# Kernel optimization log

Hardware: AMD Instinct MI355X
Metric: run time of the kernel (lower is better)

The kernel has to match this reference:

```python
import jax, jax.numpy as jnp
import numpy as np

N_NODES = 100000
N_EDGES = 1600000
D_IN = 64
D_OUT = 64


def setup_inputs() -> dict:
    key = jax.random.key(0)
    k1, k2, k3, k4 = jax.random.split(key, 4)
    x = jax.random.normal(k1, (N_NODES, D_IN), dtype=jnp.float32)
    W = jax.random.normal(k2, (D_OUT, D_IN), dtype=jnp.float32) * 0.1
    b = jax.random.normal(k3, (D_OUT,), dtype=jnp.float32) * 0.1
    edge_index = jax.random.randint(k4, (2, N_EDGES), 0, N_NODES, dtype=jnp.int64 if jax.config.jax_enable_x64 else jnp.int32)
    return {"x": x, "W": W, "b": b, "edge_index": edge_index}


def reference(x, W, b, edge_index):
    N = x.shape[0]
    # add self loops
    loop = jnp.arange(N, dtype=edge_index.dtype)
    src = jnp.concatenate([edge_index[0], loop])  # row: source nodes
    dst = jnp.concatenate([edge_index[1], loop])  # col: target nodes
    E = src.shape[0]

    # linear transform
    h = x @ W.T + b  # [N, D_OUT]

    # degree over source (row) indices, as in the original message()
    ones = jnp.ones((E,), dtype=h.dtype)
    deg = jax.ops.segment_sum(ones, src, num_segments=N)  # [N]
    deg_inv_sqrt = jnp.where(deg > 0, jax.lax.rsqrt(jnp.maximum(deg, 1.0)), 0.0)
    norm = deg_inv_sqrt[src] * deg_inv_sqrt[dst]  # [E]

    # gather-scale messages, then scatter-mean into targets
    msg = norm[:, None] * h[src]  # [E, D_OUT]
    agg_sum = jax.ops.segment_sum(msg, dst, num_segments=N)  # [N, D_OUT]
    cnt = jax.ops.segment_sum(ones, dst, num_segments=N)  # [N]
    out = agg_sum / jnp.maximum(cnt, 1.0)[:, None]
    return out
```

## Files before the change

### kernel.cpp

```cpp
#include <hip/hip_runtime.h>
#include <hip/hip_fp16.h>

#define N_D 64
#define PB_D 5
#define PSZ_D 32
#define CAP_D 768
#define SCAP  1024
#define GCAP  (SCAP / 8)
#define PB_S 7
#define PSZ_S 128
#define CAP_S 3072

__global__ __launch_bounds__(1024) void scatter_kernel(const int* __restrict__ src,
                                                       const int* __restrict__ dst,
                                                       int* __restrict__ cursorD,
                                                       int* __restrict__ cursorS,
                                                       unsigned* __restrict__ epart,
                                                       unsigned char* __restrict__ spart,
                                                       int E, int PD, int PS) {
    extern __shared__ int sh[];
    int* hD = sh;
    int* hS = sh + PD;
    int* bD = sh + PD + PS;
    int* bS = sh + 2 * PD + PS;
    int t = threadIdx.x;
    for (int i = t; i < PD + PS; i += 1024) sh[i] = 0;
    __syncthreads();
    const int4* src4 = (const int4*)src;
    const int4* dst4 = (const int4*)dst;
    int E4 = E >> 2;
    int per = (E4 + gridDim.x - 1) / gridDim.x;
    int beg = blockIdx.x * per, end = min(E4, beg + per);
    bool tailblk = (blockIdx.x == 0);
    for (int e = beg + t; e < end; e += 1024) {
        int4 d = dst4[e];
        int4 s = src4[e];
        atomicAdd(&hD[d.x >> PB_D], 1);
        atomicAdd(&hD[d.y >> PB_D], 1);
        atomicAdd(&hD[d.z >> PB_D], 1);
        atomicAdd(&hD[d.w >> PB_D], 1);
        atomicAdd(&hS[s.x >> PB_S], 1);
        atomicAdd(&hS[s.y >> PB_S], 1);
        atomicAdd(&hS[s.z >> PB_S], 1);
        atomicAdd(&hS[s.w >> PB_S], 1);
    }
    if (tailblk) {
        for (int e = (E4 << 2) + t; e < E; e += 1024) {
            atomicAdd(&hD[dst[e] >> PB_D], 1);
            atomicAdd(&hS[src[e] >> PB_S], 1);
        }
    }
    __syncthreads();
    for (int p = t; p < PD; p += 1024) {
        int hd = hD[p];
        if (hd) {
            int r = atomicAdd(&cursorD[p], hd);
            if (r > CAP_D - hd) r = max(CAP_D - hd, 0);
            bD[p] = r;
        }
        hD[p] = 0;
    }
    for (int p = t; p < PS; p += 1024) {
        int hs_ = hS[p];
        if (hs_) {
            int r = atomicAdd(&cursorS[p], hs_);
            if (r > CAP_S - hs_) r = max(CAP_S - hs_, 0);
            bS[p] = r;
        }
        hS[p] = 0;
    }
    __syncthreads();
    for (int e = beg + t; e < end; e += 1024) {
        int4 dv = dst4[e];
        int4 sv = src4[e];
        int ds_[4] = {dv.x, dv.y, dv.z, dv.w};
        int ss_[4] = {sv.x, sv.y, sv.z, sv.w};
#pragma unroll
        for (int k = 0; k < 4; k++) {
            int d = ds_[k], s0 = ss_[k];
            int pd = d >> PB_D, ps = s0 >> PB_S;
            int od = atomicAdd(&hD[pd], 1);
            epart[(size_t)pd * CAP_D + bD[pd] + od] =
                ((unsigned)s0 << PB_D) | (unsigned)(d & (PSZ_D - 1));
            int os = atomicAdd(&hS[ps], 1);
            spart[(size_t)ps * CAP_S + bS[ps] + os] = (unsigned char)(s0 & (PSZ_S - 1));
        }
    }
    if (tailblk) {
        for (int e = (E4 << 2) + t; e < E; e += 1024) {
            int d = dst[e], s0 = src[e];
            int pd = d >> PB_D, ps = s0 >> PB_S;
            int od = atomicAdd(&hD[pd], 1);
            epart[(size_t)pd * CAP_D + bD[pd] + od] =
                ((unsigned)s0 << PB_D) | (unsigned)(d & (PSZ_D - 1));
            int os = atomicAdd(&hS[ps], 1);
            spart[(size_t)ps * CAP_S + bS[ps] + os] = (unsigned char)(s0 & (PSZ_S - 1));
        }
    }
}

#define LROWS 128
__global__ __launch_bounds__(256) void linear_kernel(const float* __restrict__ x,
                                                     const float* __restrict__ W,
                                                     const float* __restrict__ b,
                                                     const unsigned char* __restrict__ spart,
                                                     const int* __restrict__ cursorS,
                                                     float* __restrict__ dis,
                                                     __half* __restrict__ hs, int N) {
    __shared__ float xs[LROWS][N_D + 1];
    __shared__ float Wt[N_D][N_D + 4];
    __shared__ float bs[N_D];
    __shared__ int ohist[PSZ_S];
    __shared__ float disS[PSZ_S];

    int tid = threadIdx.x;
    int p = blockIdx.x;
    if (p == 0 && tid < 32) ((int*)hs)[(size_t)N * 32 + tid] = 0;
    if (tid < PSZ_S) ohist[tid] = 0;
    for (int i = tid; i < N_D * N_D; i += 256) {
        int o = i >> 6, k = i & 63;
        Wt[k][o] = W[i];
    }
    if (tid < N_D) bs[tid] = b[tid];
    __syncthreads();

    {
        size_t sbase = (size_t)p * CAP_S;
        int len = min(cursorS[p], CAP_S);
        const unsigned* sp4 = (const unsigned*)(spart + sbase);
        int n4 = len >> 2;
        for (int i = tid; i < n4; i += 256) {
            unsigned v = sp4[i];
            atomicAdd(&ohist[v & 127], 1);
            atomicAdd(&ohist[(v >> 8) & 127], 1);
            atomicAdd(&ohist[(v >> 16) & 127], 1);
            atomicAdd(&ohist[(v >> 24) & 127], 1);
        }
        for (int i = (n4 << 2) + tid; i < len; i += 256)
            atomicAdd(&ohist[spart[sbase + i]], 1);
    }

    int row0 = p * LROWS;
    const float4* x4 = (const float4*)(x + (size_t)row0 * N_D);
    const int n4x = LROWS * N_D / 4;
    if (row0 + LROWS <= N) {
        for (int i = tid; i < n4x; i += 256) {
            float4 v = x4[i];
            int r = i >> 4, kq = (i & 15) << 2;
            xs[r][kq] = v.x; xs[r][kq + 1] = v.y; xs[r][kq + 2] = v.z; xs[r][kq + 3] = v.w;
        }
    } else {
        for (int i = tid; i < n4x; i += 256) {
            int r = i >> 4, kq = (i & 15) << 2;
            float4 v = make_float4(0.f, 0.f, 0.f, 0.f);
            if (row0 + r < N) v = x4[i];
            xs[r][kq] = v.x; xs[r][kq + 1] = v.y; xs[r][kq + 2] = v.z; xs[r][kq + 3] = v.w;
        }
    }
    __syncthreads();

    if (tid < PSZ_S) {
        float dv = rsqrtf((float)(ohist[tid] + 1));
        disS[tid] = dv;
        int node = row0 + tid;
        if (node < N) dis[node] = dv;
    }
    __syncthreads();

    int tc = tid >> 5;
    int tr = tid & 31;
    float acc[4][8];
#pragma unroll
    for (int j = 0; j < 4; j++)
#pragma unroll
        for (int i = 0; i < 8; i++) acc[j][i] = 0.f;

#pragma unroll 4
    for (int k = 0; k < N_D; k++) {
        float4 w0 = *(const float4*)&Wt[k][tc * 8];
        float4 w1 = *(const float4*)&Wt[k][tc * 8 + 4];
        float wv[8] = {w0.x, w0.y, w0.z, w0.w, w1.x, w1.y, w1.z, w1.w};
        float xv[4];
#pragma unroll
        for (int j = 0; j < 4; j++) xv[j] = xs[tr + 32 * j][k];
#pragma unroll
        for (int j = 0; j < 4; j++)
#pragma unroll
            for (int i = 0; i < 8; i++) acc[j][i] += xv[j] * wv[i];
    }

#pragma unroll
    for (int j = 0; j < 4; j++) {
        int row = row0 + tr + 32 * j;
        if (row < N) {
            float dr = disS[tr + 32 * j];
            union { __half h[8]; int4 v; } u;
#pragma unroll
            for (int i = 0; i < 8; i++)
                u.h[i] = __float2half_rn((acc[j][i] + bs[tc * 8 + i]) * dr);
            *(int4*)(hs + (size_t)row * N_D + tc * 8) = u.v;
        }
    }
}

__device__ __forceinline__ void acc8(int4 v, float* a) {
    union { int i; __half2 h; } u;
    float2 f;
    u.i = v.x; f = __half22float2(u.h); a[0] += f.x; a[1] += f.y;
    u.i = v.y; f = __half22float2(u.h); a[2] += f.x; a[3] += f.y;
    u.i = v.z; f = __half22float2(u.h); a[4] += f.x; a[5] += f.y;
    u.i = v.w; f = __half22float2(u.h); a[6] += f.x; a[7] += f.y;
}

__global__ __launch_bounds__(256) void gather_part_kernel(const unsigned* __restrict__ epart,
                                                          const int* __restrict__ cursorD,
                                                          const __half* __restrict__ hs,
                                                          const float* __restrict__ dis,
                                                          float* __restrict__ out, int N) {
    __shared__ unsigned raw[CAP_D];
    __shared__ int sorted[SCAP];
    __shared__ int hist[PSZ_D];
    __shared__ int rs[PSZ_D];
    __shared__ int cur[PSZ_D];
    __shared__ short gnode[GCAP + 8];
    __shared__ float disL[PSZ_D];
    int p = blockIdx.x, t = threadIdx.x;
    if (t < PSZ_D) hist[t] = 0;
    __syncthreads();
    size_t base = (size_t)p * CAP_D;
    int num = min(cursorD[p], CAP_D);
    {
        const uint4* ep4 = (const uint4*)(epart + base);
        int n4 = num >> 2;
        for (int i4 = t; i4 < n4; i4 += 256) {
            uint4 v = ep4[i4];
            ((uint4*)raw)[i4] = v;
            atomicAdd(&hist[v.x & (PSZ_D - 1)], 1);
            atomicAdd(&hist[v.y & (PSZ_D - 1)], 1);
            atomicAdd(&hist[v.z & (PSZ_D - 1)], 1);
            atomicAdd(&hist[v.w & (PSZ_D - 1)], 1);
        }
        for (int i = (n4 << 2) + t; i < num; i += 256) {
            unsigned e = epart[base + i];
            raw[i] = e;
            atomicAdd(&hist[e & (PSZ_D - 1)], 1);
        }
    }
    __syncthreads();
    if (t < PSZ_D) {
        int v = (hist[t] + 8) & ~7;
        int s = v;
#pragma unroll
        for (int off = 1; off < PSZ_D; off <<= 1) {
            int n = __shfl_up(s, off, 64);
            if (t >= off) s += n;
        }
        int ex = s - v;
        rs[t] = ex;
        cur[t] = ex;
        int cnt = hist[t];
        int node = (p << PB_D) + t;
        int pb = ex + cnt;
        int pad = ((cnt + 8) & ~7) - cnt;
        const int ZERO_OFF = N << 7;
        sorted[pb] = (node < N) ? (node << 7) : ZERO_OFF;
        for (int k = 1; k < pad; k++) sorted[pb + k] = ZERO_OFF;
        int g0 = ex >> 3, g1 = (ex + cnt + pad) >> 3;
        for (int G = g0; G < g1; ++G) gnode[G] = (short)t;
        if (t == PSZ_D - 1) gnode[g1] = -1;
        disL[t] = (node < N) ? dis[node] : 0.f;
    }
    __syncthreads();
    for (int i = t; i < num; i += 256) {
        unsigned e = raw[i];
        int pos = atomicAdd(&cur[e & (PSZ_D - 1)], 1);
        sorted[pos] = (int)((e & ~(unsigned)(PSZ_D - 1)) << 2);
    }
    __syncthreads();

    int w = t >> 6, lane = t & 63;
    int g = lane & 7, q = lane >> 3;
    int qb = q << 4;
    const char* hbase = (const char*)hs;
    int r0 = w * 8;
    int rlast = r0 + 7;
    int G = rs[r0] >> 3;
    int gend = (rs[rlast] + ((hist[rlast] + 8) & ~7)) >> 3;
    int r = r0;
    float a[8];
#pragma unroll
    for (int i = 0; i < 8; i++) a[i] = 0.f;

    auto proc = [&](int4 v, int Gi) {
        acc8(v, a);
        int nr = gnode[Gi + 1];
        if (nr != r) {
#pragma unroll
            for (int m = 1; m <= 4; m <<= 1)
#pragma unroll
                for (int i = 0; i < 8; i++) a[i] += __shfl_xor(a[i], m, 64);
            int node = (p << PB_D) + r;
            float scale = disL[r] / (float)(hist[r] + 1);
            if (g == 0 && node < N) {
                float4* op = (float4*)(out + ((size_t)node << 6) + (q << 3));
                op[0] = make_float4(a[0] * scale, a[1] * scale, a[2] * scale, a[3] * scale);
                op[1] = make_float4(a[4] * scale, a[5] * scale, a[6] * scale, a[7] * scale);
            }
#pragma unroll
            for (int i = 0; i < 8; i++) a[i] = 0.f;
            r = nr;
        }
    };

    while (G + 8 <= gend) {
        int o0 = sorted[(G + 0) * 8 + g] + qb;
        int o1 = sorted[(G + 1) * 8 + g] + qb;
        int o2 = sorted[(G + 2) * 8 + g] + qb;
        int o3 = sorted[(G + 3) * 8 + g] + qb;
        int o4 = sorted[(G + 4) * 8 + g] + qb;
        int o5 = sorted[(G + 5) * 8 + g] + qb;
        int o6 = sorted[(G + 6) * 8 + g] + qb;
        int o7 = sorted[(G + 7) * 8 + g] + qb;
        int4 v0 = *(const int4*)(hbase + (size_t)(unsigned)o0);
        int4 v1 = *(const int4*)(hbase + (size_t)(unsigned)o1);
        int4 v2 = *(const int4*)(hbase + (size_t)(unsigned)o2);
        int4 v3 = *(const int4*)(hbase + (size_t)(unsigned)o3);
        int4 v4 = *(const int4*)(hbase + (size_t)(unsigned)o4);
        int4 v5 = *(const int4*)(hbase + (size_t)(unsigned)o5);
        int4 v6 = *(const int4*)(hbase + (size_t)(unsigned)o6);
        int4 v7 = *(const int4*)(hbase + (size_t)(unsigned)o7);
        proc(v0, G + 0);
        proc(v1, G + 1);
        proc(v2, G + 2);
        proc(v3, G + 3);
        proc(v4, G + 4);
        proc(v5, G + 5);
        proc(v6, G + 6);
        proc(v7, G + 7);
        G += 8;
    }
    while (G < gend) {
        int o = sorted[G * 8 + g] + qb;
        int4 v = *(const int4*)(hbase + (size_t)(unsigned)o);
        proc(v, G);
        ++G;
    }
}

extern "C" void kernel_launch(void* const* d_in, const int* in_sizes, int n_in,
                              void* d_out, int out_size, void* d_ws, size_t ws_size,
                              hipStream_t stream) {
    const float* x = (const float*)d_in[0];
    const float* W = (const float*)d_in[1];
    const float* b = (const float*)d_in[2];
    const int* edge_index = (const int*)d_in[3];

    const int N = in_sizes[0] / N_D;
    const int E = in_sizes[3] / 2;
    const int* src = edge_index;
    const int* dst = edge_index + E;
    float* out = (float*)d_out;

    const int PD = (N + PSZ_D - 1) / PSZ_D;
    const int PS = (N + PSZ_S - 1) / PSZ_S;

    char* ws = (char*)d_ws;
    size_t off = 0;
    __half* hs = (__half*)(ws + off);         off += ((size_t)(N + 1) * N_D * sizeof(__half) + 15) & ~15ull;
    float* dis = (float*)(ws + off);          off += (size_t)N * sizeof(float);
    unsigned* epart = (unsigned*)(ws + off);  off += (size_t)PD * CAP_D * sizeof(unsigned);
    unsigned char* spart = (unsigned char*)(ws + off); off += (size_t)PS * CAP_S;
    int* cursorD = (int*)(ws + off);          off += (size_t)PD * sizeof(int);
    int* cursorS = (int*)(ws + off);          off += (size_t)PS * sizeof(int);
    (void)ws_size;

    size_t lds_scat = 2u * (PD + PS) * sizeof(int);

    hipMemsetAsync(cursorD, 0, (size_t)(PD + PS) * sizeof(int), stream);

    scatter_kernel<<<256, 1024, lds_scat, stream>>>(src, dst, cursorD, cursorS,
                                                    epart, spart, E, PD, PS);
    linear_kernel<<<PS, 256, 0, stream>>>(x, W, b, spart, cursorS, dis, hs, N);
    gather_part_kernel<<<PD, 256, 0, stream>>>(epart, cursorD, hs, dis, out, N);
}
```

Measured before the change: 190.0 us.

## Fuse scatter, linear and gather stages into one cooperative persistent kernel

Replaces the memset and three separate kernel launches with a single cooperative kernel that separates the phases with grid.sync and reuses one shared-memory union across them. Cursor zeroing moves inside the kernel, and the histogram pass is split from the reserve pass by a grid barrier. The linear and gather stages become persistent sweeps over partitions, and each 1024-thread block handles eight gather partitions at once through 128-thread sub-groups. The aim is to remove launch gaps and the memset, at the cost of grid-wide barriers, lower occupancy from the large LDS footprint, and possible load imbalance.

```diff
diff --git a/kernel.cpp b/kernel.cpp
--- a/kernel.cpp
+++ b/kernel.cpp
@@ -1,5 +1,8 @@
 #include <hip/hip_runtime.h>
 #include <hip/hip_fp16.h>
+#include <hip/hip_cooperative_groups.h>
+
+namespace cg = cooperative_groups;
 
 #define N_D 64
 #define PB_D 5
@@ -10,340 +13,355 @@
 #define PB_S 7
 #define PSZ_S 128
 #define CAP_S 3072
-
-__global__ __launch_bounds__(1024) void scatter_kernel(const int* __restrict__ src,
-                                                       const int* __restrict__ dst,
-                                                       int* __restrict__ cursorD,
-                                                       int* __restrict__ cursorS,
-                                                       unsigned* __restrict__ epart,
-                                                       unsigned char* __restrict__ spart,
-                                                       int E, int PD, int PS) {
-    extern __shared__ int sh[];
-    int* hD = sh;
-    int* hS = sh + PD;
-    int* bD = sh + PD + PS;
-    int* bS = sh + 2 * PD + PS;
-    int t = threadIdx.x;
-    for (int i = t; i < PD + PS; i += 1024) sh[i] = 0;
-    __syncthreads();
-    const int4* src4 = (const int4*)src;
-    const int4* dst4 = (const int4*)dst;
-    int E4 = E >> 2;
-    int per = (E4 + gridDim.x - 1) / gridDim.x;
-    int beg = blockIdx.x * per, end = min(E4, beg + per);
-    bool tailblk = (blockIdx.x == 0);
-    for (int e = beg + t; e < end; e += 1024) {
-        int4 d = dst4[e];
-        int4 s = src4[e];
-        atomicAdd(&hD[d.x >> PB_D], 1);
-        atomicAdd(&hD[d.y >> PB_D], 1);
-        atomicAdd(&hD[d.z >> PB_D], 1);
-        atomicAdd(&hD[d.w >> PB_D], 1);
-        atomicAdd(&hS[s.x >> PB_S], 1);
-        atomicAdd(&hS[s.y >> PB_S], 1);
-        atomicAdd(&hS[s.z >> PB_S], 1);
-        atomicAdd(&hS[s.w >> PB_S], 1);
+#define LROWS 128
+#define NTHR 1024
+#define PD_C 3125
+#define PS_C 782
+
+struct GatSub {
+    unsigned raw[CAP_D];
+    int sorted[SCAP];
+    int hist[PSZ_D];
+    int rs[PSZ_D];
+    int cur[PSZ_D];
+    short gnode[GCAP + 8];
+    float disL[PSZ_D];
+};
+
+union SharedU {
+    int scat[2 * (PD_C + PS_C)];
+    struct {
+        float xs[LROWS][N_D + 1];
+        float Wt[N_D][N_D + 4];
+        float bs[N_D];
+        int ohist[PSZ_S];
+        float disS[PSZ_S];
+    } lin;
+    struct {
+        GatSub sub[8];
+    } gat;
+};
+
+__global__ __launch_bounds__(NTHR, 8) void fused_kernel(
+    const float* __restrict__ x, const float* __restrict__ W, const float* __restrict__ bias,
+    const int* __restrict__ src, const int* __restrict__ dst, int E, int N, int PD, int PS,
+    unsigned* __restrict__ epart, unsigned char* __restrict__ spart,
+    int* __restrict__ cursorD, int* __restrict__ cursorS,
+    float* __restrict__ dis, __half* __restrict__ hs, float* __restrict__ out) {
+    __shared__ SharedU sh;
+    cg::grid_group grid = cg::this_grid();
+    const int t = threadIdx.x;
+    const int blk = blockIdx.x;
+    const int nb = gridDim.x;
+
+    {
+        int* hD = sh.scat;
+        int* hS = sh.scat + PD;
+        int* bD = sh.scat + PD + PS;
+        int* bS = sh.scat + 2 * PD + PS;
+        for (int i = t; i < PD + PS; i += NTHR) sh.scat[i] = 0;
+        for (int i = blk * NTHR + t; i < PD; i += nb * NTHR) cursorD[i] = 0;
+        for (int i = blk * NTHR + t; i < PS; i += nb * NTHR) cursorS[i] = 0;
+        __syncthreads();
+        const int4* src4 = (const int4*)src;
+        const int4* dst4 = (const int4*)dst;
+        int E4 = E >> 2;
+        int per = (E4 + nb - 1) / nb;
+        int beg = blk * per, end = min(E4, beg + per);
+        bool tailblk = (blk == 0);
+        for (int e = beg + t; e < end; e += NTHR) {
+            int4 d = dst4[e];
+            int4 s = src4[e];
+            atomicAdd(&hD[d.x >> PB_D], 1);
+            atomicAdd(&hD[d.y >> PB_D], 1);
+            atomicAdd(&hD[d.z >> PB_D], 1);
+            atomicAdd(&hD[d.w >> PB_D], 1);
+            atomicAdd(&hS[s.x >> PB_S], 1);
+            atomicAdd(&hS[s.y >> PB_S], 1);
+            atomicAdd(&hS[s.z >> PB_S], 1);
+            atomicAdd(&hS[s.w >> PB_S], 1);
+        }
+        if (tailblk) {
+            for (int e = (E4 << 2) + t; e < E; e += NTHR) {
+                atomicAdd(&hD[dst[e] >> PB_D], 1);
+                atomicAdd(&hS[src[e] >> PB_S], 1);
+            }
+        }
+        __syncthreads();
+        __threadfence();
+        grid.sync();
+        for (int p = t; p < PD; p += NTHR) {
+            int hd = hD[p];
+            if (hd) {
+                int r = atomicAdd(&cursorD[p], hd);
+                if (r > CAP_D - hd) r = max(CAP_D - hd, 0);
+                bD[p] = r;
+            }
+            hD[p] = 0;
+        }
+        for (int p = t; p < PS; p += NTHR) {
+            int hs_ = hS[p];
+            if (hs_) {
+                int r = atomicAdd(&cursorS[p], hs_);
+                if (r > CAP_S - hs_) r = max(CAP_S - hs_, 0);
+                bS[p] = r;
+            }
+            hS[p] = 0;
+        }
+        __syncthreads();
+        for (int e = beg + t; e < end; e += NTHR) {
+            int4 dv = dst4[e];
+            int4 sv = src4[e];
+            int ds_[4] = {dv.x, dv.y, dv.z, dv.w};
+            int ss_[4] = {sv.x, sv.y, sv.z, sv.w};
+#pragma unroll
+            for (int k = 0; k < 4; k++) {
+                int d = ds_[k], s0 = ss_[k];
+                int pd = d >> PB_D, ps = s0 >> PB_S;
+                int od = atomicAdd(&hD[pd], 1);
+                epart[(size_t)pd * CAP_D + bD[pd] + od] =
+                    ((unsigned)s0 << PB_D) | (unsigned)(d & (PSZ_D - 1));
+                int os = atomicAdd(&hS[ps], 1);
+                spart[(size_t)ps * CAP_S + bS[ps] + os] = (unsigned char)(s0 & (PSZ_S - 1));
+            }
+        }
+        if (tailblk) {
+            for (int e = (E4 << 2) + t; e < E; e += NTHR) {
+                int d = dst[e], s0 = src[e];
+                int pd = d >> PB_D, ps = s0 >> PB_S;
+                int od = atomicAdd(&hD[pd], 1);
+                epart[(size_t)pd * CAP_D + bD[pd] + od] =
+                    ((unsigned)s0 << PB_D) | (unsigned)(d & (PSZ_D - 1));
+                int os = atomicAdd(&hS[ps], 1);
+                spart[(size_t)ps * CAP_S + bS[ps] + os] = (unsigned char)(s0 & (PSZ_S - 1));
+            }
+        }
     }
-    if (tailblk) {
-        for (int e = (E4 << 2) + t; e < E; e += 1024) {
-            atomicAdd(&hD[dst[e] >> PB_D], 1);
-            atomicAdd(&hS[src[e] >> PB_S], 1);
+    __threadfence();
+    grid.sync();
+
+    {
+        if (blk == 0 && t < 32) ((int*)hs)[(size_t)N * 32 + t] = 0;
+        for (int i = t; i < N_D * N_D; i += NTHR) {
+            int o = i >> 6, k = i & 63;
+            sh.lin.Wt[k][o] = W[i];
+        }
+        if (t < N_D) sh.lin.bs[t] = bias[t];
+        int sweepsL = (PS + nb - 1) / nb;
+        for (int s = 0; s < sweepsL; s++) {
+            int pt = s * nb + blk;
+            bool act = pt < PS;
+            if (t < PSZ_S) sh.lin.ohist[t] = 0;
+            __syncthreads();
+            int row0 = pt * LROWS;
+            if (act) {
+                size_t sbase = (size_t)pt * CAP_S;
+                int len = min(cursorS[pt], CAP_S);
+                const unsigned* sp4 = (const unsigned*)(spart + sbase);
+                int n4 = len >> 2;
+                for (int i = t; i < n4; i += NTHR) {
+                    unsigned v = sp4[i];
+                    atomicAdd(&sh.lin.ohist[v & 127], 1);
+                    atomicAdd(&sh.lin.ohist[(v >> 8) & 127], 1);
+                    atomicAdd(&sh.lin.ohist[(v >> 16) & 127], 1);
+                    atomicAdd(&sh.lin.ohist[(v >> 24) & 127], 1);
+                }
+                for (int i = (n4 << 2) + t; i < len; i += NTHR)
+                    atomicAdd(&sh.lin.ohist[spart[sbase + i]], 1);
+                const float4* x4 = (const float4*)(x + (size_t)row0 * N_D);
+                for (int i = t; i < LROWS * N_D / 4; i += NTHR) {
+                    int r = i >> 4, kq = (i & 15) << 2;
+                    float4 v = make_float4(0.f, 0.f, 0.f, 0.f);
+                    if (row0 + r < N) v = x4[i];
+                    sh.lin.xs[r][kq] = v.x;
+                    sh.lin.xs[r][kq + 1] = v.y;
+                    sh.lin.xs[r][kq + 2] = v.z;
+                    sh.lin.xs[r][kq + 3] = v.w;
+                }
+            }
+            __syncthreads();
+            if (act && t < PSZ_S) {
+                float dv = 0.f;
+                int node = row0 + t;
+                if (node < N) {
+                    dv = rsqrtf((float)(sh.lin.ohist[t] + 1));
+                    dis[node] = dv;
+                }
+                sh.lin.disS[t] = dv;
+            }
+            __syncthreads();
+            if (act) {
+                int tc = t >> 7;
+                int tr = t & 127;
+                float acc[8];
+#pragma unroll
+                for (int i = 0; i < 8; i++) acc[i] = 0.f;
+#pragma unroll 4
+                for (int k = 0; k < N_D; k++) {
+                    float xv = sh.lin.xs[tr][k];
+                    float4 w0 = *(const float4*)&sh.lin.Wt[k][tc * 8];
+                    float4 w1 = *(const float4*)&sh.lin.Wt[k][tc * 8 + 4];
+                    acc[0] += xv * w0.x; acc[1] += xv * w0.y;
+                    acc[2] += xv * w0.z; acc[3] += xv * w0.w;
+                    acc[4] += xv * w1.x; acc[5] += xv * w1.y;
+                    acc[6] += xv * w1.z; acc[7] += xv * w1.w;
+                }
+                int row = row0 + tr;
+                if (row < N) {
+                    float dr = sh.lin.disS[tr];
+                    union { __half h[8]; int4 v; } u;
+#pragma unroll
+                    for (int i = 0; i < 8; i++)
+                        u.h[i] = __float2half_rn((acc[i] + sh.lin.bs[tc * 8 + i]) * dr);
+                    *(int4*)(hs + (size_t)row * N_D + tc * 8) = u.v;
+                }
+            }
+            __syncthreads();
         }
     }
-    __syncthreads();
-    for (int p = t; p < PD; p += 1024) {
-        int hd = hD[p];
-        if (hd) {
-            int r = atomicAdd(&cursorD[p], hd);
-            if (r > CAP_D - hd) r = max(CAP_D - hd, 0);
-            bD[p] = r;
-        }
-        hD[p] = 0;
-    }
-    for (int p = t; p < PS; p += 1024) {
-        int hs_ = hS[p];
-        if (hs_) {
-            int r = atomicAdd(&cursorS[p], hs_);
-            if (r > CAP_S - hs_) r = max(CAP_S - hs_, 0);
-            bS[p] = r;
-        }
-        hS[p] = 0;
-    }
-    __syncthreads();
-    for (int e = beg + t; e < end; e += 1024) {
-        int4 dv = dst4[e];
-        int4 sv = src4[e];
-        int ds_[4] = {dv.x, dv.y, dv.z, dv.w};
-        int ss_[4] = {sv.x, sv.y, sv.z, sv.w};
-#pragma unroll
-        for (int k = 0; k < 4; k++) {
-            int d = ds_[k], s0 = ss_[k];
-            int pd = d >> PB_D, ps = s0 >> PB_S;
-            int od = atomicAdd(&hD[pd], 1);
-            epart[(size_t)pd * CAP_D + bD[pd] + od] =
-                ((unsigned)s0 << PB_D) | (unsigned)(d & (PSZ_D - 1));
-            int os = atomicAdd(&hS[ps], 1);
-            spart[(size_t)ps * CAP_S + bS[ps] + os] = (unsigned char)(s0 & (PSZ_S - 1));
-        }
-    }
-    if (tailblk) {
-        for (int e = (E4 << 2) + t; e < E; e += 1024) {
-            int d = dst[e], s0 = src[e];
-            int pd = d >> PB_D, ps = s0 >> PB_S;
-            int od = atomicAdd(&hD[pd], 1);
-            epart[(size_t)pd * CAP_D + bD[pd] + od] =
-                ((unsigned)s0 << PB_D) | (unsigned)(d & (PSZ_D - 1));
-            int os = atomicAdd(&hS[ps], 1);
-            spart[(size_t)ps * CAP_S + bS[ps] + os] = (unsigned char)(s0 & (PSZ_S - 1));
-        }
-    }
-}
-
-#define LROWS 128
-__global__ __launch_bounds__(256) void linear_kernel(const float* __restrict__ x,
-                                                     const float* __restrict__ W,
-                                                     const float* __restrict__ b,
-                                                     const unsigned char* __restrict__ spart,
-                                                     const int* __restrict__ cursorS,
-                                                     float* __restrict__ dis,
-                                                     __half* __restrict__ hs, int N) {
-    __shared__ float xs[LROWS][N_D + 1];
-    __shared__ float Wt[N_D][N_D + 4];
-    __shared__ float bs[N_D];
-    __shared__ int ohist[PSZ_S];
-    __shared__ float disS[PSZ_S];
-
-    int tid = threadIdx.x;
-    int p = blockIdx.x;
-    if (p == 0 && tid < 32) ((int*)hs)[(size_t)N * 32 + tid] = 0;
-    if (tid < PSZ_S) ohist[tid] = 0;
-    for (int i = tid; i < N_D * N_D; i += 256) {
-        int o = i >> 6, k = i & 63;
-        Wt[k][o] = W[i];
-    }
-    if (tid < N_D) bs[tid] = b[tid];
-    __syncthreads();
+    __threadfence();
+    grid.sync();
 
     {
-        size_t sbase = (size_t)p * CAP_S;
-        int len = min(cursorS[p], CAP_S);
-        const unsigned* sp4 = (const unsigned*)(spart + sbase);
-        int n4 = len >> 2;
-        for (int i = tid; i < n4; i += 256) {
-            unsigned v = sp4[i];
-            atomicAdd(&ohist[v & 127], 1);
-            atomicAdd(&ohist[(v >> 8) & 127], 1);
-            atomicAdd(&ohist[(v >> 16) & 127], 1);
-            atomicAdd(&ohist[(v >> 24) & 127], 1);
-        }
-        for (int i = (n4 << 2) + tid; i < len; i += 256)
-            atomicAdd(&ohist[spart[sbase + i]], 1);
-    }
-
-    int row0 = p * LROWS;
-    const float4* x4 = (const float4*)(x + (size_t)row0 * N_D);
-    const int n4x = LROWS * N_D / 4;
-    if (row0 + LROWS <= N) {
-        for (int i = tid; i < n4x; i += 256) {
-            float4 v = x4[i];
-            int r = i >> 4, kq = (i & 15) << 2;
-            xs[r][kq] = v.x; xs[r][kq + 1] = v.y; xs[r][kq + 2] = v.z; xs[r][kq + 3] = v.w;
-        }
-    } else {
-        for (int i = tid; i < n4x; i += 256) {
-            int r = i >> 4, kq = (i & 15) << 2;
-            float4 v = make_float4(0.f, 0.f, 0.f, 0.f);
-            if (row0 + r < N) v = x4[i];
-            xs[r][kq] = v.x; xs[r][kq + 1] = v.y; xs[r][kq + 2] = v.z; xs[r][kq + 3] = v.w;
-        }
-    }
-    __syncthreads();
-
-    if (tid < PSZ_S) {
-        float dv = rsqrtf((float)(ohist[tid] + 1));
-        disS[tid] = dv;
-        int node = row0 + tid;
-        if (node < N) dis[node] = dv;
-    }
-    __syncthreads();
-
-    int tc = tid >> 5;
-    int tr = tid & 31;
-    float acc[4][8];
-#pragma unroll
-    for (int j = 0; j < 4; j++)
-#pragma unroll
-        for (int i = 0; i < 8; i++) acc[j][i] = 0.f;
-
-#pragma unroll 4
-    for (int k = 0; k < N_D; k++) {
-        float4 w0 = *(const float4*)&Wt[k][tc * 8];
-        float4 w1 = *(const float4*)&Wt[k][tc * 8 + 4];
-        float wv[8] = {w0.x, w0.y, w0.z, w0.w, w1.x, w1.y, w1.z, w1.w};
-        float xv[4];
-#pragma unroll
-        for (int j = 0; j < 4; j++) xv[j] = xs[tr + 32 * j][k];
-#pragma unroll
-        for (int j = 0; j < 4; j++)
-#pragma unroll
-            for (int i = 0; i < 8; i++) acc[j][i] += xv[j] * wv[i];
-    }
-
-#pragma unroll
-    for (int j = 0; j < 4; j++) {
-        int row = row0 + tr + 32 * j;
-        if (row < N) {
-            float dr = disS[tr + 32 * j];
-            union { __half h[8]; int4 v; } u;
-#pragma unroll
-            for (int i = 0; i < 8; i++)
-                u.h[i] = __float2half_rn((acc[j][i] + bs[tc * 8 + i]) * dr);
-            *(int4*)(hs + (size_t)row * N_D + tc * 8) = u.v;
-        }
-    }
-}
-
-__device__ __forceinline__ void acc8(int4 v, float* a) {
-    union { int i; __half2 h; } u;
-    float2 f;
-    u.i = v.x; f = __half22float2(u.h); a[0] += f.x; a[1] += f.y;
-    u.i = v.y; f = __half22float2(u.h); a[2] += f.x; a[3] += f.y;
-    u.i = v.z; f = __half22float2(u.h); a[4] += f.x; a[5] += f.y;
-    u.i = v.w; f = __half22float2(u.h); a[6] += f.x; a[7] += f.y;
-}
-
-__global__ __launch_bounds__(256) void gather_part_kernel(const unsigned* __restrict__ epart,
-                                                          const int* __restrict__ cursorD,
-                                                          const __half* __restrict__ hs,
-                                                          const float* __restrict__ dis,
-                                                          float* __restrict__ out, int N) {
-    __shared__ unsigned raw[CAP_D];
-    __shared__ int sorted[SCAP];
-    __shared__ int hist[PSZ_D];
-    __shared__ int rs[PSZ_D];
-    __shared__ int cur[PSZ_D];
-    __shared__ short gnode[GCAP + 8];
-    __shared__ float disL[PSZ_D];
-    int p = blockIdx.x, t = threadIdx.x;
-    if (t < PSZ_D) hist[t] = 0;
-    __syncthreads();
-    size_t base = (size_t)p * CAP_D;
-    int num = min(cursorD[p], CAP_D);
-    {
-        const uint4* ep4 = (const uint4*)(epart + base);
-        int n4 = num >> 2;
-        for (int i4 = t; i4 < n4; i4 += 256) {
-            uint4 v = ep4[i4];
-            ((uint4*)raw)[i4] = v;
-            atomicAdd(&hist[v.x & (PSZ_D - 1)], 1);
-            atomicAdd(&hist[v.y & (PSZ_D - 1)], 1);
-            atomicAdd(&hist[v.z & (PSZ_D - 1)], 1);
-            atomicAdd(&hist[v.w & (PSZ_D - 1)], 1);
-        }
-        for (int i = (n4 << 2) + t; i < num; i += 256) {
-            unsigned e = epart[base + i];
-            raw[i] = e;
-            atomicAdd(&hist[e & (PSZ_D - 1)], 1);
-        }
-    }
-    __syncthreads();
-    if (t < PSZ_D) {
-        int v = (hist[t] + 8) & ~7;
-        int s = v;
-#pragma unroll
-        for (int off = 1; off < PSZ_D; off <<= 1) {
-            int n = __shfl_up(s, off, 64);
-            if (t >= off) s += n;
-        }
-        int ex = s - v;
-        rs[t] = ex;
-        cur[t] = ex;
-        int cnt = hist[t];
-        int node = (p << PB_D) + t;
-        int pb = ex + cnt;
-        int pad = ((cnt + 8) & ~7) - cnt;
-        const int ZERO_OFF = N << 7;
-        sorted[pb] = (node < N) ? (node << 7) : ZERO_OFF;
-        for (int k = 1; k < pad; k++) sorted[pb + k] = ZERO_OFF;
-        int g0 = ex >> 3, g1 = (ex + cnt + pad) >> 3;
-        for (int G = g0; G < g1; ++G) gnode[G] = (short)t;
-        if (t == PSZ_D - 1) gnode[g1] = -1;
-        disL[t] = (node < N) ? dis[node] : 0.f;
-    }
-    __syncthreads();
-    for (int i = t; i < num; i += 256) {
-        unsigned e = raw[i];
-        int pos = atomicAdd(&cur[e & (PSZ_D - 1)], 1);
-        sorted[pos] = (int)((e & ~(unsigned)(PSZ_D - 1)) << 2);
-    }
-    __syncthreads();
-
-    int w = t >> 6, lane = t & 63;
-    int g = lane & 7, q = lane >> 3;
-    int qb = q << 4;
-    const char* hbase = (const char*)hs;
-    int r0 = w * 8;
-    int rlast = r0 + 7;
-    int G = rs[r0] >> 3;
-    int gend = (rs[rlast] + ((hist[rlast] + 8) & ~7)) >> 3;
-    int r = r0;
-    float a[8];
-#pragma unroll
-    for (int i = 0; i < 8; i++) a[i] = 0.f;
-
-    auto proc = [&](int4 v, int Gi) {
-        acc8(v, a);
-        int nr = gnode[Gi + 1];
-        if (nr != r) {
-#pragma unroll
-            for (int m = 1; m <= 4; m <<= 1)
-#pragma unroll
-                for (int i = 0; i < 8; i++) a[i] += __shfl_xor(a[i], m, 64);
-            int node = (p << PB_D) + r;
-            float scale = disL[r] / (float)(hist[r] + 1);
-            if (g == 0 && node < N) {
-                float4* op = (float4*)(out + ((size_t)node << 6) + (q << 3));
-                op[0] = make_float4(a[0] * scale, a[1] * scale, a[2] * scale, a[3] * scale);
-                op[1] = make_float4(a[4] * scale, a[5] * scale, a[6] * scale, a[7] * scale);
-            }
-#pragma unroll
-            for (int i = 0; i < 8; i++) a[i] = 0.f;
-            r = nr;
-        }
-    };
-
-    while (G + 8 <= gend) {
-        int o0 = sorted[(G + 0) * 8 + g] + qb;
-        int o1 = sorted[(G + 1) * 8 + g] + qb;
-        int o2 = sorted[(G + 2) * 8 + g] + qb;
-        int o3 = sorted[(G + 3) * 8 + g] + qb;
-        int o4 = sorted[(G + 4) * 8 + g] + qb;
-        int o5 = sorted[(G + 5) * 8 + g] + qb;
-        int o6 = sorted[(G + 6) * 8 + g] + qb;
-        int o7 = sorted[(G + 7) * 8 + g] + qb;
-        int4 v0 = *(const int4*)(hbase + (size_t)(unsigned)o0);
-        int4 v1 = *(const int4*)(hbase + (size_t)(unsigned)o1);
-        int4 v2 = *(const int4*)(hbase + (size_t)(unsigned)o2);
-        int4 v3 = *(const int4*)(hbase + (size_t)(unsigned)o3);
-        int4 v4 = *(const int4*)(hbase + (size_t)(unsigned)o4);
-        int4 v5 = *(const int4*)(hbase + (size_t)(unsigned)o5);
-        int4 v6 = *(const int4*)(hbase + (size_t)(unsigned)o6);
-        int4 v7 = *(const int4*)(hbase + (size_t)(unsigned)o7);
-        proc(v0, G + 0);
-        proc(v1, G + 1);
-        proc(v2, G + 2);
-        proc(v3, G + 3);
-        proc(v4, G + 4);
-        proc(v5, G + 5);
-        proc(v6, G + 6);
-        proc(v7, G + 7);
-        G += 8;
-    }
-    while (G < gend) {
-        int o = sorted[G * 8 + g] + qb;
-        int4 v = *(const int4*)(hbase + (size_t)(unsigned)o);
-        proc(v, G);
-        ++G;
+        int sub = t >> 7;
+        int ts = t & 127;
+        GatSub* gs = &sh.gat.sub[sub];
+        int slots = nb * 8;
+        int sweepsG = (PD + slots - 1) / slots;
+        const char* hbase = (const char*)hs;
+        for (int s = 0; s < sweepsG; s++) {
+            int p = (s * nb + blk) * 8 + sub;
+            bool act = p < PD;
+            if (ts < PSZ_D) gs->hist[ts] = 0;
+            __syncthreads();
+            size_t base = (size_t)p * CAP_D;
+            int num = 0;
+            if (act) {
+                num = min(cursorD[p], CAP_D);
+                const uint4* ep4 = (const uint4*)(epart + base);
+                int n4 = num >> 2;
+                for (int i4 = ts; i4 < n4; i4 += 128) {
+                    uint4 v = ep4[i4];
+                    ((uint4*)gs->raw)[i4] = v;
+                    atomicAdd(&gs->hist[v.x & (PSZ_D - 1)], 1);
+                    atomicAdd(&gs->hist[v.y & (PSZ_D - 1)], 1);
+                    atomicAdd(&gs->hist[v.z & (PSZ_D - 1)], 1);
+                    atomicAdd(&gs->hist[v.w & (PSZ_D - 1)], 1);
+                }
+                for (int i = (n4 << 2) + ts; i < num; i += 128) {
+                    unsigned e = epart[base + i];
+                    gs->raw[i] = e;
+                    atomicAdd(&gs->hist[e & (PSZ_D - 1)], 1);
+                }
+            }
+            __syncthreads();
+            if (act && ts < PSZ_D) {
+                int v = (gs->hist[ts] + 8) & ~7;
+                int s_ = v;
+#pragma unroll
+                for (int off = 1; off < PSZ_D; off <<= 1) {
+                    int n = __shfl_up(s_, off, 64);
+                    if (ts >= off) s_ += n;
+                }
+                int ex = s_ - v;
+                gs->rs[ts] = ex;
+                gs->cur[ts] = ex;
+                int cnt = gs->hist[ts];
+                int node = (p << PB_D) + ts;
+                int pb = ex + cnt;
+                int pad = ((cnt + 8) & ~7) - cnt;
+                const int ZERO_OFF = N << 7;
+                gs->sorted[pb] = (node < N) ? (node << 7) : ZERO_OFF;
+                for (int k = 1; k < pad; k++) gs->sorted[pb + k] = ZERO_OFF;
+                int g0 = ex >> 3, g1 = (ex + cnt + pad) >> 3;
+                for (int G2 = g0; G2 < g1; ++G2) gs->gnode[G2] = (short)ts;
+                if (ts == PSZ_D - 1) gs->gnode[g1] = -1;
+                gs->disL[ts] = (node < N) ? dis[node] : 0.f;
+            }
+            __syncthreads();
+            if (act) {
+                for (int i = ts; i < num; i += 128) {
+                    unsigned e = gs->raw[i];
+                    int pos = atomicAdd(&gs->cur[e & (PSZ_D - 1)], 1);
+                    gs->sorted[pos] = (int)((e & ~(unsigned)(PSZ_D - 1)) << 2);
+                }
+            }
+            __syncthreads();
+            if (act) {
+                int lane = ts & 63;
+                int w = ts >> 6;
+                int g = lane & 7, q = lane >> 3;
+                int qb = q << 4;
+                int r0 = w * 16, rlast = r0 + 15;
+                int G = gs->rs[r0] >> 3;
+                int gend = (gs->rs[rlast] + ((gs->hist[rlast] + 8) & ~7)) >> 3;
+                int r = r0;
+                float a[8];
+#pragma unroll
+                for (int i = 0; i < 8; i++) a[i] = 0.f;
+
+                auto proc = [&](int4 v, int Gi) {
+                    union { int i; __half2 h; } u;
+                    float2 f;
+                    u.i = v.x; f = __half22float2(u.h); a[0] += f.x; a[1] += f.y;
+                    u.i = v.y; f = __half22float2(u.h); a[2] += f.x; a[3] += f.y;
+                    u.i = v.z; f = __half22float2(u.h); a[4] += f.x; a[5] += f.y;
+                    u.i = v.w; f = __half22float2(u.h); a[6] += f.x; a[7] += f.y;
+                    int nr = gs->gnode[Gi + 1];
+                    if (nr != r) {
+#pragma unroll
+                        for (int m = 1; m <= 4; m <<= 1)
+#pragma unroll
+                            for (int i = 0; i < 8; i++) a[i] += __shfl_xor(a[i], m, 64);
+                        int node = (p << PB_D) + r;
+                        float scale = gs->disL[r] / (float)(gs->hist[r] + 1);
+                        if (g == 0 && node < N) {
+                            float4* op = (float4*)(out + ((size_t)node << 6) + (q << 3));
+                            op[0] = make_float4(a[0] * scale, a[1] * scale, a[2] * scale, a[3] * scale);
+                            op[1] = make_float4(a[4] * scale, a[5] * scale, a[6] * scale, a[7] * scale);
+                        }
+#pragma unroll
+                        for (int i = 0; i < 8; i++) a[i] = 0.f;
+                        r = nr;
+                    }
+                };
+
+                while (G + 8 <= gend) {
+                    int o0 = gs->sorted[(G + 0) * 8 + g] + qb;
+                    int o1 = gs->sorted[(G + 1) * 8 + g] + qb;
+                    int o2 = gs->sorted[(G + 2) * 8 + g] + qb;
+                    int o3 = gs->sorted[(G + 3) * 8 + g] + qb;
+                    int o4 = gs->sorted[(G + 4) * 8 + g] + qb;
+                    int o5 = gs->sorted[(G + 5) * 8 + g] + qb;
+                    int o6 = gs->sorted[(G + 6) * 8 + g] + qb;
+                    int o7 = gs->sorted[(G + 7) * 8 + g] + qb;
+                    int4 v0 = *(const int4*)(hbase + (size_t)(unsigned)o0);
+                    int4 v1 = *(const int4*)(hbase + (size_t)(unsigned)o1);
+                    int4 v2 = *(const int4*)(hbase + (size_t)(unsigned)o2);
+                    int4 v3 = *(const int4*)(hbase + (size_t)(unsigned)o3);
+                    int4 v4 = *(const int4*)(hbase + (size_t)(unsigned)o4);
+                    int4 v5 = *(const int4*)(hbase + (size_t)(unsigned)o5);
+                    int4 v6 = *(const int4*)(hbase + (size_t)(unsigned)o6);
+                    int4 v7 = *(const int4*)(hbase + (size_t)(unsigned)o7);
+                    proc(v0, G + 0);
+                    proc(v1, G + 1);
+                    proc(v2, G + 2);
+                    proc(v3, G + 3);
+                    proc(v4, G + 4);
+                    proc(v5, G + 5);
+                    proc(v6, G + 6);
+                    proc(v7, G + 7);
+                    G += 8;
+                }
+                while (G < gend) {
+                    int o = gs->sorted[G * 8 + g] + qb;
+                    int4 v = *(const int4*)(hbase + (size_t)(unsigned)o);
+                    proc(v, G);
+                    ++G;
+                }
+            }
+            __syncthreads();
+        }
     }
 }
 
@@ -355,14 +373,14 @@
     const float* b = (const float*)d_in[2];
     const int* edge_index = (const int*)d_in[3];
 
-    const int N = in_sizes[0] / N_D;
-    const int E = in_sizes[3] / 2;
+    int N = in_sizes[0] / N_D;
+    int E = in_sizes[3] / 2;
     const int* src = edge_index;
     const int* dst = edge_index + E;
     float* out = (float*)d_out;
 
-    const int PD = (N + PSZ_D - 1) / PSZ_D;
-    const int PS = (N + PSZ_S - 1) / PSZ_S;
+    int PD = (N + PSZ_D - 1) / PSZ_D;
+    int PS = (N + PSZ_S - 1) / PSZ_S;
 
     char* ws = (char*)d_ws;
     size_t off = 0;
@@ -374,12 +392,18 @@
     int* cursorS = (int*)(ws + off);          off += (size_t)PS * sizeof(int);
     (void)ws_size;
 
-    size_t lds_scat = 2u * (PD + PS) * sizeof(int);
-
-    hipMemsetAsync(cursorD, 0, (size_t)(PD + PS) * sizeof(int), stream);
-
-    scatter_kernel<<<256, 1024, lds_scat, stream>>>(src, dst, cursorD, cursorS,
-                                                    epart, spart, E, PD, PS);
-    linear_kernel<<<PS, 256, 0, stream>>>(x, W, b, spart, cursorS, dis, hs, N);
-    gather_part_kernel<<<PD, 256, 0, stream>>>(epart, cursorD, hs, dis, out, N);
+    static int mb = -1;
+    if (mb < 0) {
+        int q = 0;
+        hipError_t err = hipOccupancyMaxActiveBlocksPerMultiprocessor(&q, fused_kernel, NTHR, 0);
+        mb = (err == hipSuccess && q >= 1) ? q : 1;
+    }
+    int grid = mb * 256;
+    if (grid > 512) grid = 512;
+
+    void* args[] = {(void*)&x, (void*)&W, (void*)&b, (void*)&src, (void*)&dst,
+                    (void*)&E, (void*)&N, (void*)&PD, (void*)&PS,
+                    (void*)&epart, (void*)&spart, (void*)&cursorD, (void*)&cursorS,
+                    (void*)&dis, (void*)&hs, (void*)&out};
+    hipLaunchCooperativeKernel((void*)fused_kernel, dim3(grid), dim3(NTHR), args, 0, stream);
 }
```

New measurement: 604.6 us. 218% more time.
